# Kernel tuning notes

Measured on AMD Instinct MI355X. Metric: run time of the kernel, lower is better.

The kernel has to match this reference:

```python
import jax, jax.numpy as jnp
import numpy as np

B, L, D, H, F, NL, K, G = 2, 2048, 768, 12, 3072, 12, 128, 16
HD = D // H
SCALE = HD ** -0.5


def setup_inputs() -> dict:
    key = jax.random.key(0)
    ks = jax.random.split(key, 8)
    n = lambda k, s, std=0.02: jax.random.normal(k, s, dtype=jnp.float32) * std
    return {
        "x": jax.random.normal(ks[0], (B, L, D), dtype=jnp.float32),
        "pos_conv_w": n(ks[1], (D, D // G, K)),
        "pos_conv_b": jnp.zeros((D,), jnp.float32),
        "ln0_g": jnp.ones((D,), jnp.float32), "ln0_b": jnp.zeros((D,), jnp.float32),
        "Wq": n(ks[2], (NL, D, D)), "bq": jnp.zeros((NL, D), jnp.float32),
        "Wk": n(ks[3], (NL, D, D)), "bk": jnp.zeros((NL, D), jnp.float32),
        "Wv": n(ks[4], (NL, D, D)), "bv": jnp.zeros((NL, D), jnp.float32),
        "Wo": n(ks[5], (NL, D, D)), "bo": jnp.zeros((NL, D), jnp.float32),
        "ln1_g": jnp.ones((NL, D), jnp.float32), "ln1_b": jnp.zeros((NL, D), jnp.float32),
        "W1": n(ks[6], (NL, D, F)), "b1": jnp.zeros((NL, F), jnp.float32),
        "W2": n(ks[7], (NL, F, D)), "b2": jnp.zeros((NL, D), jnp.float32),
        "ln2_g": jnp.ones((NL, D), jnp.float32), "ln2_b": jnp.zeros((NL, D), jnp.float32),
    }


def _ln(x, g, b, eps=1e-5):
    m = jnp.mean(x, axis=-1, keepdims=True)
    v = jnp.mean(jnp.square(x - m), axis=-1, keepdims=True)
    return (x - m) * jax.lax.rsqrt(v + eps) * g + b


def reference(x, pos_conv_w, pos_conv_b, ln0_g, ln0_b, Wq, bq, Wk, bk, Wv, bv, Wo, bo,
              ln1_g, ln1_b, W1, b1, W2, b2, ln2_g, ln2_b):
    b_, l_, d_ = x.shape
    # positional grouped conv embedding (kernel even -> drop last frame), GELU, residual add
    pos = jax.lax.conv_general_dilated(x.transpose(0, 2, 1), pos_conv_w, (1,), [(K // 2, K // 2)],
                                       feature_group_count=G)  # (B, D, L+1)
    pos = pos[:, :, :l_] + pos_conv_b[None, :, None]
    h = x + jax.nn.gelu(pos, approximate=False).transpose(0, 2, 1)
    # post-norm encoder (layer_norm_first=False): LN applied before the layer stack
    h = _ln(h, ln0_g, ln0_b)

    def layer(h, p):
        wq, bq_, wk, bk_, wv, bv_, wo, bo_, g1, be1, w1, bf1, w2, bf2, g2, be2 = p
        r = h
        q = (h @ wq + bq_).reshape(b_, l_, H, HD)
        k = (h @ wk + bk_).reshape(b_, l_, H, HD)
        v = (h @ wv + bv_).reshape(b_, l_, H, HD)
        w = jax.nn.softmax(SCALE * jnp.einsum('blhd,bmhd->bhlm', q, k), axis=-1)
        o = jnp.einsum('bhlm,bmhd->blhd', w, v).reshape(b_, l_, d_)
        h = r + (o @ wo + bo_)
        h = _ln(h, g1, be1)
        ff = jax.nn.gelu(h @ w1 + bf1, approximate=False) @ w2 + bf2
        h = _ln(h + ff, g2, be2)
        return h, None

    h, _ = jax.lax.scan(layer, h, (Wq, bq, Wk, bk, Wv, bv, Wo, bo,
                                   ln1_g, ln1_b, W1, b1, W2, b2, ln2_g, ln2_b))
    return h
```

## Files before the change

### kernel.cpp

```cpp
#include <hip/hip_runtime.h>
#include <hip/hip_bf16.h>
#include <stdint.h>

#define B_ 2
#define L_ 2048
#define D_ 768
#define H_ 12
#define F_ 3072
#define NL_ 12
#define K_ 128
#define G_ 16
#define HD_ 64
#define CPG_ 48
#define M_TOK (B_*L_)
#define SCALE_ 0.125f

typedef __hip_bfloat16 bf16;
typedef __bf16 bf16x8 __attribute__((ext_vector_type(8)));
typedef float f32x4 __attribute__((ext_vector_type(4)));

__device__ __forceinline__ void gload16(const void* g, void* l) {
  __builtin_amdgcn_global_load_lds((const __attribute__((address_space(1))) void*)g,
                                   (__attribute__((address_space(3))) void*)l, 16, 0, 0);
}

__global__ __launch_bounds__(256) void convw_kernel(const float* __restrict__ w,
                                                    bf16* __restrict__ wT2) {
  int idx = blockIdx.x * 256 + threadIdx.x;
  int ci = idx & 63;
  int row = idx >> 6;
  int d = row % 48;
  int t2 = row / 48;
  int kk = t2 & 127;
  int g = t2 >> 7;
  float v = (ci < 48) ? w[(((size_t)(g * 48 + d) * 48) + ci) * 128 + kk] : 0.f;
  wT2[idx] = __float2bfloat16(v);
}

__global__ __launch_bounds__(256) void conv_mfma(const float* __restrict__ x,
                                                 const bf16* __restrict__ wT2,
                                                 const float* __restrict__ bias,
                                                 float* __restrict__ out) {
  const int l0 = blockIdx.x * 64, g = blockIdx.y, b = blockIdx.z;
  const int tid = threadIdx.x, w = tid >> 6, lane = tid & 63;
  const int c15 = lane & 15, g4 = lane >> 4;
  __shared__ __align__(16) bf16 win[192 * 72];
  __shared__ __align__(16) bf16 Wl[2 * 48 * 64];

  if (tid < 192) {
    int lg = l0 - 64 + tid;
    char* dst = (char*)win + tid * 144;
    uint4 z4 = {0u, 0u, 0u, 0u};
    if ((unsigned)lg < 2048u) {
      const float* srow = x + ((size_t)(b * 2048 + lg) * 768 + g * 48);
#pragma unroll
      for (int c = 0; c < 6; ++c) {
        float4 v0 = *(const float4*)(srow + c * 8);
        float4 v1 = *(const float4*)(srow + c * 8 + 4);
        union { bf16 h[8]; uint4 u; } uu;
        uu.h[0] = __float2bfloat16(v0.x); uu.h[1] = __float2bfloat16(v0.y);
        uu.h[2] = __float2bfloat16(v0.z); uu.h[3] = __float2bfloat16(v0.w);
        uu.h[4] = __float2bfloat16(v1.x); uu.h[5] = __float2bfloat16(v1.y);
        uu.h[6] = __float2bfloat16(v1.z); uu.h[7] = __float2bfloat16(v1.w);
        *(uint4*)(dst + c * 16) = uu.u;
      }
    } else {
#pragma unroll
      for (int c = 0; c < 6; ++c) *(uint4*)(dst + c * 16) = z4;
    }
    *(uint4*)(dst + 96) = z4;
    *(uint4*)(dst + 112) = z4;
  }
  __syncthreads();

  f32x4 acc[3];
  const f32x4 vzero = {0.f, 0.f, 0.f, 0.f};
  acc[0] = vzero; acc[1] = vzero; acc[2] = vzero;

  const char* wbase = (const char*)wT2 + (size_t)g * 128 * 48 * 128;

  for (int kp = 0; kp < 64; ++kp) {
#pragma unroll
    for (int i = 0; i < 3; ++i) {
      int coff = w * 3072 + i * 1024;
      int c = coff + (lane << 4);
      int row96 = c >> 7;
      int s = row96 / 48;
      int d = row96 - s * 48;
      int cb2 = c & 127;
      gload16(wbase + ((size_t)((2 * kp + s) * 48 + d)) * 128 + (cb2 ^ ((d & 7) << 4)),
              (char*)Wl + coff);
    }
    __syncthreads();
#pragma unroll
    for (int s = 0; s < 2; ++s) {
      int kk = 2 * kp + s;
#pragma unroll
      for (int cb = 0; cb < 2; ++cb) {
        bf16x8 a = *(const bf16x8*)((const char*)win + (w * 16 + c15 + kk) * 144 + cb * 64 + g4 * 16);
#pragma unroll
        for (int ct = 0; ct < 3; ++ct) {
          int d = ct * 16 + c15;
          bf16x8 bfrag = *(const bf16x8*)((const char*)Wl + s * 6144 + d * 128 +
                                          ((cb * 64 + g4 * 16) ^ ((d & 7) << 4)));
          acc[ct] = __builtin_amdgcn_mfma_f32_16x16x32_bf16(a, bfrag, acc[ct], 0, 0, 0);
        }
      }
    }
    __syncthreads();
  }

#pragma unroll
  for (int ct = 0; ct < 3; ++ct) {
    int dg = g * 48 + ct * 16 + c15;
    float bv = bias[dg];
#pragma unroll
    for (int r = 0; r < 4; ++r) {
      int l = l0 + w * 16 + g4 * 4 + r;
      size_t idx = (size_t)(b * 2048 + l) * 768 + dg;
      float vv = acc[ct][r] + bv;
      vv = 0.5f * vv * (1.0f + erff(vv * 0.70710678f));
      out[idx] = x[idx] + vv;
    }
  }
}

__global__ __launch_bounds__(256) void ln_kernel(const float* __restrict__ a,
                                                 const float* __restrict__ r,
                                                 const float* __restrict__ g,
                                                 const float* __restrict__ be,
                                                 float* __restrict__ out,
                                                 bf16* __restrict__ outb) {
  int row = blockIdx.x, tid = threadIdx.x;
  __shared__ float red[256];
  const float* ar = a + (size_t)row * D_;
  float vals[3];
  float s = 0.f;
#pragma unroll
  for (int i = 0; i < 3; ++i) {
    int c = tid + i * 256;
    float vv = ar[c];
    if (r) vv += r[(size_t)row * D_ + c];
    vals[i] = vv; s += vv;
  }
  red[tid] = s; __syncthreads();
  for (int st = 128; st > 0; st >>= 1) {
    if (tid < st) red[tid] += red[tid + st];
    __syncthreads();
  }
  float mean = red[0] * (1.0f / 768.0f);
  __syncthreads();
  float s2 = 0.f;
#pragma unroll
  for (int i = 0; i < 3; ++i) { float d2 = vals[i] - mean; s2 += d2 * d2; }
  red[tid] = s2; __syncthreads();
  for (int st = 128; st > 0; st >>= 1) {
    if (tid < st) red[tid] += red[tid + st];
    __syncthreads();
  }
  float rstd = rsqrtf(red[0] * (1.0f / 768.0f) + 1e-5f);
#pragma unroll
  for (int i = 0; i < 3; ++i) {
    int c = tid + i * 256;
    float ov = (vals[i] - mean) * rstd * g[c] + be[c];
    out[(size_t)row * D_ + c] = ov;
    if (outb) outb[(size_t)row * D_ + c] = __float2bfloat16(ov);
  }
}

__global__ __launch_bounds__(256) void castT_kernel(const float* __restrict__ src,
                                                    bf16* __restrict__ dst, int R, int C) {
  __shared__ float t[32][33];
  int c0 = blockIdx.x * 32, r0 = blockIdx.y * 32;
  int tx = threadIdx.x & 31, ty = threadIdx.x >> 5;
#pragma unroll
  for (int i = 0; i < 32; i += 8)
    t[ty + i][tx] = src[(size_t)(r0 + ty + i) * C + (c0 + tx)];
  __syncthreads();
#pragma unroll
  for (int i = 0; i < 32; i += 8)
    dst[(size_t)(c0 + ty + i) * R + (r0 + tx)] = __float2bfloat16(t[tx][ty + i]);
}

__global__ __launch_bounds__(256) void castT_qkv_kernel(const float* __restrict__ q,
                                                        const float* __restrict__ k,
                                                        const float* __restrict__ v,
                                                        bf16* __restrict__ dst) {
  int n0 = blockIdx.x * 32, k0 = blockIdx.y * 32;
  const float* src = (n0 < 768) ? q : (n0 < 1536) ? k : v;
  int nn = (n0 >= 1536) ? (n0 - 1536) : (n0 >= 768 ? n0 - 768 : n0);
  __shared__ float t[32][33];
  int tx = threadIdx.x & 31, ty = threadIdx.x >> 5;
#pragma unroll
  for (int i = 0; i < 32; i += 8)
    t[ty + i][tx] = src[(size_t)(k0 + ty + i) * 768 + nn + tx];
  __syncthreads();
#pragma unroll
  for (int i = 0; i < 32; i += 8)
    dst[(size_t)(n0 + ty + i) * 768 + k0 + tx] = __float2bfloat16(t[tx][ty + i]);
}

__global__ __launch_bounds__(256) void bcat_kernel(const float* __restrict__ bq,
                                                   const float* __restrict__ bk,
                                                   const float* __restrict__ bv,
                                                   float* __restrict__ dst) {
  int i = blockIdx.x * 256 + threadIdx.x;
  if (i >= 2304) return;
  dst[i] = (i < 768) ? bq[i] : (i < 1536) ? bk[i - 768] : bv[i - 1536];
}

__global__ __launch_bounds__(256) void vtrans_kernel(const bf16* __restrict__ qkv,
                                                     bf16* __restrict__ vT) {
  int l0 = blockIdx.x * 32, d0 = blockIdx.y * 32, bh = blockIdx.z;
  int b = bh / 12, h = bh % 12;
  __shared__ bf16 t[32][33];
  int tx = threadIdx.x & 31, ty = threadIdx.x >> 5;
#pragma unroll
  for (int i = 0; i < 32; i += 8)
    t[ty + i][tx] = qkv[(size_t)(b * 2048 + l0 + ty + i) * 2304 + 1536 + h * 64 + d0 + tx];
  __syncthreads();
#pragma unroll
  for (int i = 0; i < 32; i += 8)
    vT[((size_t)bh * 64 + d0 + ty + i) * 2048 + l0 + tx] = t[tx][ty + i];
}

template <int BM, int GELU, int BF16OUT>
__global__ __launch_bounds__(256) void gemm_bf16(const bf16* __restrict__ A,
                                                 const bf16* __restrict__ BT,
                                                 const float* __restrict__ bias,
                                                 void* __restrict__ Cout,
                                                 int N, int Kd) {
  constexpr int WM = BM / 2, MF = WM / 16;
  __shared__ bf16 As[BM * 64];
  __shared__ bf16 Bs[128 * 64];
  const int tid = threadIdx.x, w = tid >> 6, lane = tid & 63;
  int gx = gridDim.x;
  int flat = blockIdx.x + gx * blockIdx.y;
  int cpx = (gx * gridDim.y) >> 3;
  int sw = (flat & 7) * cpx + (flat >> 3);
  const int bn = sw % gx, bm = sw / gx;
  const int wr = w >> 1, wc = w & 1;
  const int c15 = lane & 15, g4 = lane >> 4;
  const int lrow8 = lane >> 3;
  const int cb = (lane & 7) * 16;

  f32x4 acc[MF][4];
  const f32x4 vzero = {0.f, 0.f, 0.f, 0.f};
#pragma unroll
  for (int i = 0; i < MF; ++i)
#pragma unroll
    for (int j = 0; j < 4; ++j) acc[i][j] = vzero;

  const char* Ab = (const char*)A;
  const char* Bb = (const char*)BT;

  for (int k0 = 0; k0 < Kd; k0 += 64) {
#pragma unroll
    for (int i = 0; i < BM / 32; ++i) {
      int t = w + 4 * i;
      int row = t * 8 + lrow8;
      gload16(Ab + ((size_t)(bm * BM + row) * Kd + k0) * 2 + (cb ^ ((row & 7) << 4)),
              (char*)As + t * 1024);
    }
#pragma unroll
    for (int i = 0; i < 4; ++i) {
      int t = w + 4 * i;
      int row = t * 8 + lrow8;
      gload16(Bb + ((size_t)(bn * 128 + row) * Kd + k0) * 2 + (cb ^ ((row & 7) << 4)),
              (char*)Bs + t * 1024);
    }
    __syncthreads();
    bf16x8 af[MF][2], bfr[4][2];
#pragma unroll
    for (int kf = 0; kf < 2; ++kf) {
      int kbyte = kf * 64 + g4 * 16;
#pragma unroll
      for (int mf = 0; mf < MF; ++mf) {
        int row = wr * WM + mf * 16 + c15;
        af[mf][kf] = *(const bf16x8*)((const char*)As + row * 128 + (kbyte ^ ((row & 7) << 4)));
      }
#pragma unroll
      for (int fn = 0; fn < 4; ++fn) {
        int row = wc * 64 + fn * 16 + c15;
        bfr[fn][kf] = *(const bf16x8*)((const char*)Bs + row * 128 + (kbyte ^ ((row & 7) << 4)));
      }
    }
    __builtin_amdgcn_s_setprio(1);
#pragma unroll
    for (int mf = 0; mf < MF; ++mf)
#pragma unroll
      for (int fn = 0; fn < 4; ++fn) {
        acc[mf][fn] = __builtin_amdgcn_mfma_f32_16x16x32_bf16(af[mf][0], bfr[fn][0], acc[mf][fn], 0, 0, 0);
        acc[mf][fn] = __builtin_amdgcn_mfma_f32_16x16x32_bf16(af[mf][1], bfr[fn][1], acc[mf][fn], 0, 0, 0);
      }
    __builtin_amdgcn_s_setprio(0);
    __syncthreads();
  }
#pragma unroll
  for (int fn = 0; fn < 4; ++fn) {
    int col = bn * 128 + wc * 64 + fn * 16 + c15;
    float bv = bias[col];
#pragma unroll
    for (int mf = 0; mf < MF; ++mf) {
#pragma unroll
      for (int r = 0; r < 4; ++r) {
        int row = bm * BM + wr * WM + mf * 16 + g4 * 4 + r;
        float vv = acc[mf][fn][r] + bv;
        if (GELU) vv = 0.5f * vv * (1.0f + erff(vv * 0.70710678f));
        if (BF16OUT) ((bf16*)Cout)[(size_t)row * N + col] = __float2bfloat16(vv);
        else        ((float*)Cout)[(size_t)row * N + col] = vv;
      }
    }
  }
}

__global__ __launch_bounds__(256) void attn_mfma(const bf16* __restrict__ qkv,
                                                 const bf16* __restrict__ vT,
                                                 bf16* __restrict__ ob) {
  int bid = blockIdx.x + 32 * (blockIdx.y + 12 * blockIdx.z);
  int wgid = (bid & 7) * 96 + (bid >> 3);
  const int q0 = (wgid & 31) * 64;
  int bh = wgid >> 5;
  const int h = bh % 12, b = bh / 12;

  const int tid = threadIdx.x, w = tid >> 6, lane = tid & 63;
  const int c15 = lane & 15, g4 = lane >> 4;
  const int lrow8 = lane >> 3;
  const int cb = (lane & 7) * 16;
  __shared__ bf16 Kl[2][4096];
  __shared__ bf16 Vl[2][4096];
  __shared__ bf16 Pl[4096];

  const f32x4 vzero = {0.f, 0.f, 0.f, 0.f};
  const char* qp = (const char*)qkv + (((size_t)(b * 2048 + q0 + w * 16 + c15)) * 2304 + h * 64) * 2;
  bf16x8 qa0 = *(const bf16x8*)(qp + g4 * 16);
  bf16x8 qa1 = *(const bf16x8*)(qp + 64 + g4 * 16);

  bf16x8 b_one;
#pragma unroll
  for (int i = 0; i < 8; ++i) b_one[i] = (__bf16)1.0f;

  f32x4 o[4], o5;
#pragma unroll
  for (int i = 0; i < 4; ++i) o[i] = vzero;
  o5 = vzero;
  float m[4] = {-1e30f, -1e30f, -1e30f, -1e30f};
  const float SC2 = 0.18033688f;
  const float THR = 11.54f;

  const char* kgb = (const char*)qkv + (((size_t)(b * 2048)) * 2304 + 768 + h * 64) * 2;
  const char* vgb = (const char*)vT + ((size_t)((b * 12 + h) * 64) * 2048) * 2;
  char* Plw = (char*)Pl + w * 2048;

#define STAGE(kt, bufi)                                                                     \
  {                                                                                         \
    char* Kd = (char*)Kl[bufi];                                                             \
    char* Vd = (char*)Vl[bufi];                                                             \
    _Pragma("unroll")                                                                       \
    for (int i = 0; i < 2; ++i) {                                                           \
      int t = w + 4 * i;                                                                    \
      int rr = t * 8 + lrow8;                                                               \
      gload16(kgb + (size_t)((kt) * 64 + rr) * 4608 + (cb ^ ((rr & 7) << 4)), Kd + t * 1024);\
      gload16(vgb + (size_t)rr * 4096 + (size_t)(kt) * 128 + (cb ^ ((rr & 7) << 4)), Vd + t * 1024);\
    }                                                                                       \
  }

  STAGE(0, 0);
  __syncthreads();

  for (int kt = 0; kt < 32; ++kt) {
    int cur = kt & 1;
    if (kt + 1 < 32) STAGE(kt + 1, cur ^ 1);

    const char* Kc = (const char*)Kl[cur];
    const char* Vc = (const char*)Vl[cur];

    f32x4 sc[4];
    __builtin_amdgcn_s_setprio(1);
#pragma unroll
    for (int fn = 0; fn < 4; ++fn) {
      int key = fn * 16 + c15;
      const char* kr = Kc + key * 128;
      int sw = (key & 7) << 4;
      bf16x8 kb0 = *(const bf16x8*)(kr + ((g4 * 16) ^ sw));
      bf16x8 kb1 = *(const bf16x8*)(kr + ((64 + g4 * 16) ^ sw));
      f32x4 s = __builtin_amdgcn_mfma_f32_16x16x32_bf16(qa0, kb0, vzero, 0, 0, 0);
      s = __builtin_amdgcn_mfma_f32_16x16x32_bf16(qa1, kb1, s, 0, 0, 0);
      sc[fn] = s;
    }
    __builtin_amdgcn_s_setprio(0);

    float pm[4];
    int ok = 1;
#pragma unroll
    for (int r = 0; r < 4; ++r) {
      pm[r] = fmaxf(fmaxf(sc[0][r], sc[1][r]), fmaxf(sc[2][r], sc[3][r]));
      ok &= (pm[r] * SC2 <= m[r] + THR) ? 1 : 0;
    }

    if (!__all(ok)) {
#pragma unroll
      for (int r = 0; r < 4; ++r) {
        float tm = pm[r];
        tm = fmaxf(tm, __shfl_xor(tm, 1));
        tm = fmaxf(tm, __shfl_xor(tm, 2));
        tm = fmaxf(tm, __shfl_xor(tm, 4));
        tm = fmaxf(tm, __shfl_xor(tm, 8));
        float mn = fmaxf(m[r], tm * SC2);
        float alpha = exp2f(m[r] - mn);
        m[r] = mn;
        o[0][r] *= alpha; o[1][r] *= alpha; o[2][r] *= alpha; o[3][r] *= alpha;
        o5[r] *= alpha;
      }
    }

#pragma unroll
    for (int r = 0; r < 4; ++r) {
      int row = g4 * 4 + r;
      int swp = (row & 7) << 4;
      char* pr = Plw + row * 128;
#pragma unroll
      for (int fn = 0; fn < 4; ++fn) {
        float p = exp2f(fmaf(sc[fn][r], SC2, -m[r]));
        int colb = (fn * 16 + c15) * 2;
        *(bf16*)(pr + (colb ^ swp)) = __float2bfloat16(p);
      }
    }

    {
      const char* pr = Plw + c15 * 128;
      int sw = (c15 & 7) << 4;
      bf16x8 pa0 = *(const bf16x8*)(pr + ((g4 * 16) ^ sw));
      bf16x8 pa1 = *(const bf16x8*)(pr + ((64 + g4 * 16) ^ sw));
      __builtin_amdgcn_s_setprio(1);
#pragma unroll
      for (int fh = 0; fh < 4; ++fh) {
        int hd = fh * 16 + c15;
        const char* vr = Vc + hd * 128;
        int swv = (hd & 7) << 4;
        bf16x8 vb0 = *(const bf16x8*)(vr + ((g4 * 16) ^ swv));
        bf16x8 vb1 = *(const bf16x8*)(vr + ((64 + g4 * 16) ^ swv));
        o[fh] = __builtin_amdgcn_mfma_f32_16x16x32_bf16(pa0, vb0, o[fh], 0, 0, 0);
        o[fh] = __builtin_amdgcn_mfma_f32_16x16x32_bf16(pa1, vb1, o[fh], 0, 0, 0);
      }
      o5 = __builtin_amdgcn_mfma_f32_16x16x32_bf16(pa0, b_one, o5, 0, 0, 0);
      o5 = __builtin_amdgcn_mfma_f32_16x16x32_bf16(pa1, b_one, o5, 0, 0, 0);
      __builtin_amdgcn_s_setprio(0);
    }
    __syncthreads();
  }
#undef STAGE

#pragma unroll
  for (int r = 0; r < 4; ++r) {
    float inv = 1.0f / o5[r];
    size_t row = (size_t)(b * 2048 + q0 + w * 16 + g4 * 4 + r);
#pragma unroll
    for (int fh = 0; fh < 4; ++fh)
      ob[row * 768 + h * 64 + fh * 16 + c15] = __float2bfloat16(o[fh][r] * inv);
  }
}

extern "C" void kernel_launch(void* const* d_in, const int* in_sizes, int n_in,
                              void* d_out, int out_size, void* d_ws, size_t ws_size,
                              hipStream_t stream) {
  const float* x      = (const float*)d_in[0];
  const float* pcw    = (const float*)d_in[1];
  const float* pcb    = (const float*)d_in[2];
  const float* ln0_g  = (const float*)d_in[3];
  const float* ln0_b  = (const float*)d_in[4];
  const float* Wq     = (const float*)d_in[5];
  const float* bq     = (const float*)d_in[6];
  const float* Wk     = (const float*)d_in[7];
  const float* bk     = (const float*)d_in[8];
  const float* Wv     = (const float*)d_in[9];
  const float* bv     = (const float*)d_in[10];
  const float* Wo     = (const float*)d_in[11];
  const float* bo     = (const float*)d_in[12];
  const float* ln1_g  = (const float*)d_in[13];
  const float* ln1_b  = (const float*)d_in[14];
  const float* W1     = (const float*)d_in[15];
  const float* b1     = (const float*)d_in[16];
  const float* W2     = (const float*)d_in[17];
  const float* b2     = (const float*)d_in[18];
  const float* ln2_g  = (const float*)d_in[19];
  const float* ln2_b  = (const float*)d_in[20];

  const size_t MDB = (size_t)M_TOK * D_ * 4;
  char* W = (char*)d_ws;
  float* h    = (float*)W;
  float* tmp  = (float*)(W + MDB);
  char*  big  = W + 2 * MDB;
  bf16*  qkv  = (bf16*)big;
  bf16*  ff   = (bf16*)big;
  bf16*  wT2  = (bf16*)big;
  char* p = W + 2 * MDB + 25165824;
  bf16* h_bf  = (bf16*)p; p += (size_t)M_TOK * D_ * 2;
  bf16* obuf  = (bf16*)p; p += (size_t)M_TOK * D_ * 2;
  bf16* vT    = (bf16*)p; p += (size_t)M_TOK * D_ * 2;
  bf16* wqkvb = (bf16*)p; p += (size_t)2304 * 768 * 2;
  bf16* wob   = (bf16*)p; p += (size_t)768 * 768 * 2;
  bf16* w1b   = (bf16*)p; p += (size_t)3072 * 768 * 2;
  bf16* w2b   = (bf16*)p; p += (size_t)768 * 3072 * 2;
  float* bqkv = (float*)p;

  convw_kernel<<<24576, 256, 0, stream>>>(pcw, wT2);
  conv_mfma<<<dim3(32, 16, 2), 256, 0, stream>>>(x, wT2, pcb, tmp);
  ln_kernel<<<M_TOK, 256, 0, stream>>>(tmp, nullptr, ln0_g, ln0_b, h, h_bf);

  for (int l = 0; l < NL_; ++l) {
    const float* wq = Wq + (size_t)l * D_ * D_;
    const float* wk = Wk + (size_t)l * D_ * D_;
    const float* wv = Wv + (size_t)l * D_ * D_;
    const float* wo = Wo + (size_t)l * D_ * D_;
    const float* w1 = W1 + (size_t)l * D_ * F_;
    const float* w2 = W2 + (size_t)l * F_ * D_;

    castT_qkv_kernel<<<dim3(72, 24), 256, 0, stream>>>(wq, wk, wv, wqkvb);
    bcat_kernel<<<9, 256, 0, stream>>>(bq + (size_t)l * D_, bk + (size_t)l * D_, bv + (size_t)l * D_, bqkv);
    castT_kernel<<<dim3(24, 24), 256, 0, stream>>>(wo, wob, 768, 768);
    castT_kernel<<<dim3(96, 24), 256, 0, stream>>>(w1, w1b, 768, 3072);
    castT_kernel<<<dim3(24, 96), 256, 0, stream>>>(w2, w2b, 3072, 768);

    gemm_bf16<128, 0, 1><<<dim3(18, 32), 256, 0, stream>>>(h_bf, wqkvb, bqkv, qkv, 2304, 768);
    vtrans_kernel<<<dim3(64, 2, 24), 256, 0, stream>>>(qkv, vT);
    attn_mfma<<<dim3(32, 12, 2), 256, 0, stream>>>(qkv, vT, obuf);
    gemm_bf16<64, 0, 0><<<dim3(6, 64), 256, 0, stream>>>(obuf, wob, bo + (size_t)l * D_, tmp, 768, 768);
    ln_kernel<<<M_TOK, 256, 0, stream>>>(tmp, h, ln1_g + (size_t)l * D_, ln1_b + (size_t)l * D_, h, h_bf);
    gemm_bf16<128, 1, 1><<<dim3(24, 32), 256, 0, stream>>>(h_bf, w1b, b1 + (size_t)l * F_, ff, 3072, 768);
    gemm_bf16<64, 0, 0><<<dim3(6, 64), 256, 0, stream>>>(ff, w2b, b2 + (size_t)l * D_, tmp, 768, 3072);
    float* out_ln2 = (l == NL_ - 1) ? (float*)d_out : h;
    ln_kernel<<<M_TOK, 256, 0, stream>>>(tmp, h, ln2_g + (size_t)l * D_, ln2_b + (size_t)l * D_, out_ln2, h_bf);
  }
}
```

Measured before the change: 2.662 ms.

## Use wave-per-row LayerNorm, 64x64 tiles for N=768 GEMMs, transposed-score attention

After: 2.390 ms. -10.2%, faster.

```diff
diff --git a/kernel.cpp b/kernel.cpp
--- a/kernel.cpp
+++ b/kernel.cpp
@@ -131,40 +131,52 @@
                                                  const float* __restrict__ be,
                                                  float* __restrict__ out,
                                                  bf16* __restrict__ outb) {
-  int row = blockIdx.x, tid = threadIdx.x;
-  __shared__ float red[256];
-  const float* ar = a + (size_t)row * D_;
-  float vals[3];
+  int w = threadIdx.x >> 6, lane = threadIdx.x & 63;
+  size_t row = (size_t)blockIdx.x * 4 + w;
+  const float* ar = a + row * 768;
+  const float* rr = r ? r + row * 768 : nullptr;
+  float4 v[3];
   float s = 0.f;
 #pragma unroll
   for (int i = 0; i < 3; ++i) {
-    int c = tid + i * 256;
-    float vv = ar[c];
-    if (r) vv += r[(size_t)row * D_ + c];
-    vals[i] = vv; s += vv;
-  }
-  red[tid] = s; __syncthreads();
-  for (int st = 128; st > 0; st >>= 1) {
-    if (tid < st) red[tid] += red[tid + st];
-    __syncthreads();
-  }
-  float mean = red[0] * (1.0f / 768.0f);
-  __syncthreads();
+    int c = lane * 4 + i * 256;
+    float4 vv = *(const float4*)(ar + c);
+    if (rr) {
+      float4 rv = *(const float4*)(rr + c);
+      vv.x += rv.x; vv.y += rv.y; vv.z += rv.z; vv.w += rv.w;
+    }
+    v[i] = vv;
+    s += vv.x + vv.y + vv.z + vv.w;
+  }
+#pragma unroll
+  for (int st = 1; st < 64; st <<= 1) s += __shfl_xor(s, st);
+  float mean = s * (1.0f / 768.0f);
   float s2 = 0.f;
 #pragma unroll
-  for (int i = 0; i < 3; ++i) { float d2 = vals[i] - mean; s2 += d2 * d2; }
-  red[tid] = s2; __syncthreads();
-  for (int st = 128; st > 0; st >>= 1) {
-    if (tid < st) red[tid] += red[tid + st];
-    __syncthreads();
-  }
-  float rstd = rsqrtf(red[0] * (1.0f / 768.0f) + 1e-5f);
-#pragma unroll
   for (int i = 0; i < 3; ++i) {
-    int c = tid + i * 256;
-    float ov = (vals[i] - mean) * rstd * g[c] + be[c];
-    out[(size_t)row * D_ + c] = ov;
-    if (outb) outb[(size_t)row * D_ + c] = __float2bfloat16(ov);
+    float dx = v[i].x - mean, dy = v[i].y - mean, dz = v[i].z - mean, dw = v[i].w - mean;
+    s2 += dx * dx + dy * dy + dz * dz + dw * dw;
+  }
+#pragma unroll
+  for (int st = 1; st < 64; st <<= 1) s2 += __shfl_xor(s2, st);
+  float rstd = rsqrtf(s2 * (1.0f / 768.0f) + 1e-5f);
+#pragma unroll
+  for (int i = 0; i < 3; ++i) {
+    int c = lane * 4 + i * 256;
+    float4 gv = *(const float4*)(g + c);
+    float4 bv = *(const float4*)(be + c);
+    float4 ov;
+    ov.x = (v[i].x - mean) * rstd * gv.x + bv.x;
+    ov.y = (v[i].y - mean) * rstd * gv.y + bv.y;
+    ov.z = (v[i].z - mean) * rstd * gv.z + bv.z;
+    ov.w = (v[i].w - mean) * rstd * gv.w + bv.w;
+    *(float4*)(out + row * 768 + c) = ov;
+    if (outb) {
+      union { bf16 h[4]; uint2 u; } pk;
+      pk.h[0] = __float2bfloat16(ov.x); pk.h[1] = __float2bfloat16(ov.y);
+      pk.h[2] = __float2bfloat16(ov.z); pk.h[3] = __float2bfloat16(ov.w);
+      *(uint2*)(outb + row * 768 + c) = pk.u;
+    }
   }
 }
 
@@ -224,15 +236,16 @@
     vT[((size_t)bh * 64 + d0 + ty + i) * 2048 + l0 + tx] = t[tx][ty + i];
 }
 
-template <int BM, int GELU, int BF16OUT>
+template <int BM, int BN, int GELU, int BF16OUT>
 __global__ __launch_bounds__(256) void gemm_bf16(const bf16* __restrict__ A,
                                                  const bf16* __restrict__ BT,
                                                  const float* __restrict__ bias,
                                                  void* __restrict__ Cout,
                                                  int N, int Kd) {
   constexpr int WM = BM / 2, MF = WM / 16;
+  constexpr int WN = BN / 2, FN = WN / 16;
   __shared__ bf16 As[BM * 64];
-  __shared__ bf16 Bs[128 * 64];
+  __shared__ bf16 Bs[BN * 64];
   const int tid = threadIdx.x, w = tid >> 6, lane = tid & 63;
   int gx = gridDim.x;
   int flat = blockIdx.x + gx * blockIdx.y;
@@ -244,12 +257,12 @@
   const int lrow8 = lane >> 3;
   const int cb = (lane & 7) * 16;
 
-  f32x4 acc[MF][4];
+  f32x4 acc[MF][FN];
   const f32x4 vzero = {0.f, 0.f, 0.f, 0.f};
 #pragma unroll
   for (int i = 0; i < MF; ++i)
 #pragma unroll
-    for (int j = 0; j < 4; ++j) acc[i][j] = vzero;
+    for (int j = 0; j < FN; ++j) acc[i][j] = vzero;
 
   const char* Ab = (const char*)A;
   const char* Bb = (const char*)BT;
@@ -263,14 +276,14 @@
               (char*)As + t * 1024);
     }
 #pragma unroll
-    for (int i = 0; i < 4; ++i) {
+    for (int i = 0; i < BN / 32; ++i) {
       int t = w + 4 * i;
       int row = t * 8 + lrow8;
-      gload16(Bb + ((size_t)(bn * 128 + row) * Kd + k0) * 2 + (cb ^ ((row & 7) << 4)),
+      gload16(Bb + ((size_t)(bn * BN + row) * Kd + k0) * 2 + (cb ^ ((row & 7) << 4)),
               (char*)Bs + t * 1024);
     }
     __syncthreads();
-    bf16x8 af[MF][2], bfr[4][2];
+    bf16x8 af[MF][2], bfr[FN][2];
 #pragma unroll
     for (int kf = 0; kf < 2; ++kf) {
       int kbyte = kf * 64 + g4 * 16;
@@ -280,8 +293,8 @@
         af[mf][kf] = *(const bf16x8*)((const char*)As + row * 128 + (kbyte ^ ((row & 7) << 4)));
       }
 #pragma unroll
-      for (int fn = 0; fn < 4; ++fn) {
-        int row = wc * 64 + fn * 16 + c15;
+      for (int fn = 0; fn < FN; ++fn) {
+        int row = wc * WN + fn * 16 + c15;
         bfr[fn][kf] = *(const bf16x8*)((const char*)Bs + row * 128 + (kbyte ^ ((row & 7) << 4)));
       }
     }
@@ -289,7 +302,7 @@
 #pragma unroll
     for (int mf = 0; mf < MF; ++mf)
 #pragma unroll
-      for (int fn = 0; fn < 4; ++fn) {
+      for (int fn = 0; fn < FN; ++fn) {
         acc[mf][fn] = __builtin_amdgcn_mfma_f32_16x16x32_bf16(af[mf][0], bfr[fn][0], acc[mf][fn], 0, 0, 0);
         acc[mf][fn] = __builtin_amdgcn_mfma_f32_16x16x32_bf16(af[mf][1], bfr[fn][1], acc[mf][fn], 0, 0, 0);
       }
@@ -297,8 +310,8 @@
     __syncthreads();
   }
 #pragma unroll
-  for (int fn = 0; fn < 4; ++fn) {
-    int col = bn * 128 + wc * 64 + fn * 16 + c15;
+  for (int fn = 0; fn < FN; ++fn) {
+    int col = bn * BN + wc * WN + fn * 16 + c15;
     float bv = bias[col];
 #pragma unroll
     for (int mf = 0; mf < MF; ++mf) {
@@ -344,7 +357,7 @@
 #pragma unroll
   for (int i = 0; i < 4; ++i) o[i] = vzero;
   o5 = vzero;
-  float m[4] = {-1e30f, -1e30f, -1e30f, -1e30f};
+  float m = -1e30f;
   const float SC2 = 0.18033688f;
   const float THR = 11.54f;
 
@@ -384,46 +397,44 @@
       int sw = (key & 7) << 4;
       bf16x8 kb0 = *(const bf16x8*)(kr + ((g4 * 16) ^ sw));
       bf16x8 kb1 = *(const bf16x8*)(kr + ((64 + g4 * 16) ^ sw));
-      f32x4 s = __builtin_amdgcn_mfma_f32_16x16x32_bf16(qa0, kb0, vzero, 0, 0, 0);
-      s = __builtin_amdgcn_mfma_f32_16x16x32_bf16(qa1, kb1, s, 0, 0, 0);
+      f32x4 s = __builtin_amdgcn_mfma_f32_16x16x32_bf16(kb0, qa0, vzero, 0, 0, 0);
+      s = __builtin_amdgcn_mfma_f32_16x16x32_bf16(kb1, qa1, s, 0, 0, 0);
       sc[fn] = s;
     }
     __builtin_amdgcn_s_setprio(0);
 
-    float pm[4];
-    int ok = 1;
-#pragma unroll
-    for (int r = 0; r < 4; ++r) {
-      pm[r] = fmaxf(fmaxf(sc[0][r], sc[1][r]), fmaxf(sc[2][r], sc[3][r]));
-      ok &= (pm[r] * SC2 <= m[r] + THR) ? 1 : 0;
-    }
+    float pm = fmaxf(
+        fmaxf(fmaxf(fmaxf(sc[0][0], sc[0][1]), fmaxf(sc[0][2], sc[0][3])),
+              fmaxf(fmaxf(sc[1][0], sc[1][1]), fmaxf(sc[1][2], sc[1][3]))),
+        fmaxf(fmaxf(fmaxf(sc[2][0], sc[2][1]), fmaxf(sc[2][2], sc[2][3])),
+              fmaxf(fmaxf(sc[3][0], sc[3][1]), fmaxf(sc[3][2], sc[3][3]))));
+    int ok = (pm * SC2 <= m + THR) ? 1 : 0;
 
     if (!__all(ok)) {
+      float tm = pm;
+      tm = fmaxf(tm, __shfl_xor(tm, 16));
+      tm = fmaxf(tm, __shfl_xor(tm, 32));
+      float mn = fmaxf(m, tm * SC2);
+      float alpha = exp2f(m - mn);
+      m = mn;
 #pragma unroll
       for (int r = 0; r < 4; ++r) {
-        float tm = pm[r];
-        tm = fmaxf(tm, __shfl_xor(tm, 1));
-        tm = fmaxf(tm, __shfl_xor(tm, 2));
-        tm = fmaxf(tm, __shfl_xor(tm, 4));
-        tm = fmaxf(tm, __shfl_xor(tm, 8));
-        float mn = fmaxf(m[r], tm * SC2);
-        float alpha = exp2f(m[r] - mn);
-        m[r] = mn;
-        o[0][r] *= alpha; o[1][r] *= alpha; o[2][r] *= alpha; o[3][r] *= alpha;
-        o5[r] *= alpha;
-      }
-    }
-
-#pragma unroll
-    for (int r = 0; r < 4; ++r) {
-      int row = g4 * 4 + r;
-      int swp = (row & 7) << 4;
-      char* pr = Plw + row * 128;
+        float ar = __shfl(alpha, g4 * 4 + r);
+        o[0][r] *= ar; o[1][r] *= ar; o[2][r] *= ar; o[3][r] *= ar;
+        o5[r] *= ar;
+      }
+    }
+
+    {
+      char* prow = Plw + c15 * 128;
+      int swp = (c15 & 7) << 4;
 #pragma unroll
       for (int fn = 0; fn < 4; ++fn) {
-        float p = exp2f(fmaf(sc[fn][r], SC2, -m[r]));
-        int colb = (fn * 16 + c15) * 2;
-        *(bf16*)(pr + (colb ^ swp)) = __float2bfloat16(p);
+        union { bf16 hh[4]; uint2 u; } pk;
+#pragma unroll
+        for (int r = 0; r < 4; ++r)
+          pk.hh[r] = __float2bfloat16(exp2f(fmaf(sc[fn][r], SC2, -m)));
+        *(uint2*)(prow + ((fn * 32 + g4 * 8) ^ swp)) = pk.u;
       }
     }
 
@@ -506,7 +517,7 @@
 
   convw_kernel<<<24576, 256, 0, stream>>>(pcw, wT2);
   conv_mfma<<<dim3(32, 16, 2), 256, 0, stream>>>(x, wT2, pcb, tmp);
-  ln_kernel<<<M_TOK, 256, 0, stream>>>(tmp, nullptr, ln0_g, ln0_b, h, h_bf);
+  ln_kernel<<<M_TOK / 4, 256, 0, stream>>>(tmp, nullptr, ln0_g, ln0_b, h, h_bf);
 
   for (int l = 0; l < NL_; ++l) {
     const float* wq = Wq + (size_t)l * D_ * D_;
@@ -522,14 +533,14 @@
     castT_kernel<<<dim3(96, 24), 256, 0, stream>>>(w1, w1b, 768, 3072);
     castT_kernel<<<dim3(24, 96), 256, 0, stream>>>(w2, w2b, 3072, 768);
 
-    gemm_bf16<128, 0, 1><<<dim3(18, 32), 256, 0, stream>>>(h_bf, wqkvb, bqkv, qkv, 2304, 768);
+    gemm_bf16<128, 128, 0, 1><<<dim3(18, 32), 256, 0, stream>>>(h_bf, wqkvb, bqkv, qkv, 2304, 768);
     vtrans_kernel<<<dim3(64, 2, 24), 256, 0, stream>>>(qkv, vT);
     attn_mfma<<<dim3(32, 12, 2), 256, 0, stream>>>(qkv, vT, obuf);
-    gemm_bf16<64, 0, 0><<<dim3(6, 64), 256, 0, stream>>>(obuf, wob, bo + (size_t)l * D_, tmp, 768, 768);
-    ln_kernel<<<M_TOK, 256, 0, stream>>>(tmp, h, ln1_g + (size_t)l * D_, ln1_b + (size_t)l * D_, h, h_bf);
-    gemm_bf16<128, 1, 1><<<dim3(24, 32), 256, 0, stream>>>(h_bf, w1b, b1 + (size_t)l * F_, ff, 3072, 768);
-    gemm_bf16<64, 0, 0><<<dim3(6, 64), 256, 0, stream>>>(ff, w2b, b2 + (size_t)l * D_, tmp, 768, 3072);
+    gemm_bf16<64, 64, 0, 0><<<dim3(12, 64), 256, 0, stream>>>(obuf, wob, bo + (size_t)l * D_, tmp, 768, 768);
+    ln_kernel<<<M_TOK / 4, 256, 0, stream>>>(tmp, h, ln1_g + (size_t)l * D_, ln1_b + (size_t)l * D_, h, h_bf);
+    gemm_bf16<128, 128, 1, 1><<<dim3(24, 32), 256, 0, stream>>>(h_bf, w1b, b1 + (size_t)l * F_, ff, 3072, 768);
+    gemm_bf16<64, 64, 0, 0><<<dim3(12, 64), 256, 0, stream>>>(ff, w2b, b2 + (size_t)l * D_, tmp, 768, 3072);
     float* out_ln2 = (l == NL_ - 1) ? (float*)d_out : h;
-    ln_kernel<<<M_TOK, 256, 0, stream>>>(tmp, h, ln2_g + (size_t)l * D_, ln2_b + (size_t)l * D_, out_ln2, h_bf);
-  }
-}
+    ln_kernel<<<M_TOK / 4, 256, 0, stream>>>(tmp, h, ln2_g + (size_t)l * D_, ln2_b + (size_t)l * D_, out_ln2, h_bf);
+  }
+}
```
